# Optimization experiments

Measured on AMD Instinct MI355X. Metric: run time of the kernel, lower is better.

The kernel has to match this reference:

```python
import jax, jax.numpy as jnp
import numpy as np

B, L, DIN, DH, DE = 16, 128, 768, 300, 100
ALPHA = 0.2
NEG = -9e15


def setup_inputs() -> dict:
    key = jax.random.key(0)
    k = jax.random.split(key, 7)
    s = lambda fan: 1.0 / np.sqrt(fan)
    return {
        "x": jax.random.normal(k[0], (B, L, DIN), jnp.float32),
        "adj": jax.random.randint(k[1], (B, L, L), 0, 2, jnp.int32),
        "edge_embedding": jax.random.normal(k[2], (B, L, L, DE), jnp.float32),
        "W": jax.random.normal(k[3], (DIN, DH), jnp.float32) * s(DIN),
        "a": jax.random.normal(k[4], (2 * DH, 1), jnp.float32) * s(2 * DH),
        "edge_map_w": jax.random.normal(k[5], (DH, DE), jnp.float32) * s(DE),
        "edge_map_b": jnp.zeros((DH,), jnp.float32),
        "edge_lin_w": jax.random.normal(k[6], (1, DH), jnp.float32) * s(DH),
        "edge_lin_b": jnp.zeros((1,), jnp.float32),
    }


def _forward(x, edge_embedding, W, a, edge_map_w, edge_map_b, edge_lin_w, edge_lin_b, adj):
    h = x @ W  # [B, L, DH]
    # Faithful to torch: h.repeat_interleave(L, dim=2).view(B, L*L, DH) scrambles
    # features: a_input_first[b, i*L+j, d] = h[b, i, (j*DH + d) // L].
    # So e1[b,i,j] = sum_d h[b,i,(j*DH+d)//L] * a[d] = h[b,i] . V[j], with V[j,k] =
    # sum of a[d] over d where (j*DH+d)//L == k. Build V once by scatter-add.
    idx = (jnp.arange(L)[:, None] * DH + jnp.arange(DH)[None, :]) // L  # [L, DH], values in [0, DH)
    a_first = a[:DH, 0]
    V = jnp.zeros((L, DH), h.dtype).at[jnp.arange(L)[:, None], idx].add(a_first[None, :])  # [L, DH]
    e1 = jnp.einsum('bik,jk->bij', h, V)  # [B, L, L]
    # Second half: h.repeat_interleave(L, dim=0).view(...) gives plain h_j tiling.
    e2 = h @ a[DH:, 0]  # [B, L], broadcast over i
    e = jax.nn.leaky_relu(e1 + e2[:, None, :], ALPHA)  # [B, L, L]
    # Edge-weight gate (use_edge_weight == 'yes'); note torch relu result is discarded.
    em = edge_embedding @ edge_map_w.T + edge_map_b  # [B, L, L, DH]
    ew = jax.nn.sigmoid(em @ edge_lin_w.T + edge_lin_b)[..., 0]  # [B, L, L]
    e_final = e * ew
    att = jax.nn.softmax(jnp.where(adj > 0, e_final, NEG), axis=2)  # dropout off (eval)
    return h + jnp.matmul(att, h)  # residual add, concat=False


def reference(x, adj, edge_embedding, W, a, edge_map_w, edge_map_b, edge_lin_w, edge_lin_b):
    return _forward(x, edge_embedding, W, a, edge_map_w, edge_map_b, edge_lin_w, edge_lin_b, adj)
```

## Files before the change

kernel.cpp:

```cpp
#include <hip/hip_runtime.h>
#include <hip/hip_bf16.h>


#define L 128
#define DH 300
#define DIN 768
#define DE 100
#define KSL 4
#define MROWS 2048

__global__ __launch_bounds__(256) void k_small(
    const float* __restrict__ A,
    const float* __restrict__ EMW,
    const float* __restrict__ EMB,
    const float* __restrict__ ELW,
    const float* __restrict__ ELB,
    float* __restrict__ CV, float* __restrict__ C0,
    float* __restrict__ VW, int* __restrict__ VCOL)
{
    int t = threadIdx.x;
    if (blockIdx.x == 0) {
        if (t < DE) {
            float s = 0.f;
            for (int k = 0; k < DH; ++k)
                s += ELW[k] * EMW[k * DE + t];
            CV[t] = s;
        } else if (t == DE) {
            float s = 0.f;
            for (int k = 0; k < DH; ++k)
                s += ELW[k] * EMB[k];
            C0[0] = s + ELB[0];
        }
    } else {
        if (t < L) {
            int base = t * DH;
            int cm = base >> 7;
            float w0 = 0.f, w1 = 0.f, w2 = 0.f, w3 = 0.f;
            for (int j = 0; j < DH; ++j) {
                int u = ((base + j) >> 7) - cm;
                float av = A[j];
                w0 += (u == 0) ? av : 0.f;
                w1 += (u == 1) ? av : 0.f;
                w2 += (u == 2) ? av : 0.f;
                w3 += (u == 3) ? av : 0.f;
            }
            VCOL[t] = cm;
            VW[t * 4 + 0] = w0; VW[t * 4 + 1] = w1;
            VW[t * 4 + 2] = w2; VW[t * 4 + 3] = w3;
        }
    }
}

__global__ __launch_bounds__(256) void k_gemm(
    const float* __restrict__ X,
    const float* __restrict__ Wm,
    float* __restrict__ HP)
{
    __shared__ float As[32 * 33];
    __shared__ float Bs[32 * 80];
    int t = threadIdx.x;
    int ty = t >> 4, tx = t & 15;
    int r0 = blockIdx.y * 32;
    int c0 = blockIdx.x * 80;
    int kbase = blockIdx.z * (DIN / KSL);

    float acc[2][5];
#pragma unroll
    for (int r = 0; r < 2; ++r)
#pragma unroll
        for (int c = 0; c < 5; ++c) acc[r][c] = 0.f;

    for (int ks = 0; ks < DIN / KSL; ks += 32) {
        int kk = kbase + ks;
#pragma unroll
        for (int s = 0; s < 4; ++s) {
            int idx = t + 256 * s;
            int row = idx >> 5, k = idx & 31;
            As[k * 33 + row] = X[(size_t)(r0 + row) * DIN + kk + k];
        }
        for (int idx = t; idx < 640; idx += 256) {
            int k = idx / 20, c4 = idx % 20;
            int c = c4 * 4;
            int col = c0 + c;
            float4 v;
            if (col + 3 < DH) v = *(const float4*)(Wm + (size_t)(kk + k) * DH + col);
            else { v.x = 0.f; v.y = 0.f; v.z = 0.f; v.w = 0.f; }
            *(float4*)(Bs + k * 80 + c) = v;
        }
        __syncthreads();
#pragma unroll
        for (int k = 0; k < 32; ++k) {
            float av0 = As[k * 33 + ty * 2];
            float av1 = As[k * 33 + ty * 2 + 1];
            float bv[5];
#pragma unroll
            for (int c = 0; c < 5; ++c) bv[c] = Bs[k * 80 + tx * 5 + c];
#pragma unroll
            for (int c = 0; c < 5; ++c) {
                acc[0][c] = fmaf(av0, bv[c], acc[0][c]);
                acc[1][c] = fmaf(av1, bv[c], acc[1][c]);
            }
        }
        __syncthreads();
    }
    float* out = HP + (size_t)blockIdx.z * (MROWS * DH);
#pragma unroll
    for (int r = 0; r < 2; ++r) {
        int row = r0 + ty * 2 + r;
#pragma unroll
        for (int c = 0; c < 5; ++c) {
            int col = c0 + tx * 5 + c;
            if (col < DH) out[(size_t)row * DH + col] = acc[r][c];
        }
    }
}

__global__ __launch_bounds__(256) void k_red(
    const float* __restrict__ HP, const float* __restrict__ A,
    float* __restrict__ H, float* __restrict__ E2)
{
    const size_t SL = (size_t)MROWS * DH;
    int t = threadIdx.x;
    int row = blockIdx.x * 8 + (t >> 5);
    int lane = t & 31;
    const float4* p0 = (const float4*)(HP + (size_t)row * DH);
    const float4* p1 = (const float4*)(HP + SL + (size_t)row * DH);
    const float4* p2 = (const float4*)(HP + 2 * SL + (size_t)row * DH);
    const float4* p3 = (const float4*)(HP + 3 * SL + (size_t)row * DH);
    const float4* a4 = (const float4*)(A + DH);
    float4* hout = (float4*)(H + (size_t)row * DH);
    float acc = 0.f;
    for (int k4 = lane; k4 < DH / 4; k4 += 32) {
        float4 v0 = p0[k4], v1 = p1[k4], v2 = p2[k4], v3 = p3[k4];
        float4 av = a4[k4];
        float4 hv;
        hv.x = (v0.x + v1.x) + (v2.x + v3.x);
        hv.y = (v0.y + v1.y) + (v2.y + v3.y);
        hv.z = (v0.z + v1.z) + (v2.z + v3.z);
        hv.w = (v0.w + v1.w) + (v2.w + v3.w);
        hout[k4] = hv;
        acc += hv.x * av.x + hv.y * av.y + hv.z * av.z + hv.w * av.w;
    }
#pragma unroll
    for (int o = 16; o >= 1; o >>= 1) acc += __shfl_xor(acc, o);
    if (lane == 0) E2[row] = acc;
}

__global__ __launch_bounds__(256) void k_attn(
    const float* __restrict__ EE,
    const int* __restrict__ ADJ,
    const float* __restrict__ H,
    const float* __restrict__ E2,
    const float* __restrict__ CV, const float* __restrict__ C0,
    const float* __restrict__ VW, const int* __restrict__ VCOL,
    float* __restrict__ OUT)
{
    __shared__ float hrow[DH];
    __shared__ float cl[DE];
    __shared__ float ef[L];
    __shared__ float att[L];
    __shared__ float red[4];

    int bid = blockIdx.x;
    int b = bid >> 7;
    int t = threadIdx.x;

    for (int k = t; k < DH; k += 256) hrow[k] = H[(size_t)bid * DH + k];
    if (t < DE) cl[t] = CV[t];
    __syncthreads();

    {
        int j = t >> 1, half = t & 1;
        const float2* p = (const float2*)(EE + (size_t)bid * (L * DE) + j * DE + half * 50);
        const float* cp = cl + half * 50;
        float s = 0.f;
#pragma unroll
        for (int q = 0; q < 25; ++q) {
            float2 v = p[q];
            s = fmaf(v.x, cp[2 * q], s);
            s = fmaf(v.y, cp[2 * q + 1], s);
        }
        s += __shfl_xor(s, 1);
        float ewv = 1.f / (1.f + expf(-(s + C0[0])));

        int cm = VCOL[j];
        float e1 = 0.f;
#pragma unroll
        for (int u = 0; u < 4; ++u) {
            int c = cm + u; if (c > DH - 1) c = DH - 1;
            e1 += VW[j * 4 + u] * hrow[c];
        }
        float e = e1 + E2[(size_t)b * L + j];
        e = (e > 0.f) ? e : 0.2f * e;
        float efv = (ADJ[(size_t)bid * L + j] > 0) ? e * ewv : -9.0e15f;
        if (half == 0) ef[j] = efv;
    }
    __syncthreads();

    float v = (t < L) ? ef[t] : -3.0e38f;
#pragma unroll
    for (int o = 32; o >= 1; o >>= 1) v = fmaxf(v, __shfl_xor(v, o));
    int wid = t >> 6;
    if ((t & 63) == 0) red[wid] = v;
    __syncthreads();
    float mx = fmaxf(fmaxf(red[0], red[1]), fmaxf(red[2], red[3]));
    __syncthreads();
    float p = (t < L) ? expf(ef[t] - mx) : 0.f;
    v = p;
#pragma unroll
    for (int o = 32; o >= 1; o >>= 1) v += __shfl_xor(v, o);
    if ((t & 63) == 0) red[wid] = v;
    __syncthreads();
    float denom = red[0] + red[1] + red[2] + red[3];
    if (t < L) att[t] = p / denom;
    __syncthreads();

    const float* Hb = H + (size_t)b * L * DH;
    for (int k = t; k < DH; k += 256) {
        float a0 = hrow[k], a1 = 0.f, a2 = 0.f, a3 = 0.f;
#pragma unroll 4
        for (int j = 0; j < L; j += 4) {
            a0 = fmaf(att[j + 0], Hb[(size_t)(j + 0) * DH + k], a0);
            a1 = fmaf(att[j + 1], Hb[(size_t)(j + 1) * DH + k], a1);
            a2 = fmaf(att[j + 2], Hb[(size_t)(j + 2) * DH + k], a2);
            a3 = fmaf(att[j + 3], Hb[(size_t)(j + 3) * DH + k], a3);
        }
        OUT[(size_t)bid * DH + k] = (a0 + a1) + (a2 + a3);
    }
}

extern "C" void kernel_launch(void* const* d_in, const int* in_sizes, int n_in,
                              void* d_out, int out_size, void* d_ws, size_t ws_size,
                              hipStream_t stream) {
    const float* X   = (const float*)d_in[0];
    const int*   ADJ = (const int*)d_in[1];
    const float* EE  = (const float*)d_in[2];
    const float* Wm  = (const float*)d_in[3];
    const float* A   = (const float*)d_in[4];
    const float* EMW = (const float*)d_in[5];
    const float* EMB = (const float*)d_in[6];
    const float* ELW = (const float*)d_in[7];
    const float* ELB = (const float*)d_in[8];
    float* OUT = (float*)d_out;

    float* ws = (float*)d_ws;
    float* HP   = ws;
    float* H    = ws + 2457600;
    float* E2   = ws + 3072000;
    float* CV   = ws + 3074048;
    float* C0   = ws + 3074148;
    float* VW   = ws + 3074152;
    int*   VCOL = (int*)(ws + 3074664);

    k_small<<<dim3(2), dim3(256), 0, stream>>>(A, EMW, EMB, ELW, ELB, CV, C0, VW, VCOL);
    k_gemm<<<dim3(4, 64, 4), dim3(256), 0, stream>>>(X, Wm, HP);
    k_red<<<dim3(256), dim3(256), 0, stream>>>(HP, A, H, E2);
    k_attn<<<dim3(2048), dim3(256), 0, stream>>>(EE, ADJ, H, E2, CV, C0, VW, VCOL, OUT);
}
```

Baseline: 87.98 us.

## Compute x@W with bf16 MFMA using pre-transposed bf16 weights

Replaces the scalar fp32 split-K GEMM with a bf16 MFMA 16x16x32 kernel on 64x64 tiles. A new kernel transposes W and converts it to bf16 each call, and X is converted to bf16 while it is staged into shared memory. The aim is to use the matrix cores instead of FMA loops, at the cost of one extra launch and lower precision for h, which then feeds the attention scores and the output.

```diff
diff --git a/kernel.cpp b/kernel.cpp
--- a/kernel.cpp
+++ b/kernel.cpp
@@ -6,8 +6,20 @@
 #define DH 300
 #define DIN 768
 #define DE 100
-#define KSL 4
+#define SPLITK 4
 #define MROWS 2048
+#define SL ((size_t)MROWS * DH)
+
+typedef __bf16 bf16x8 __attribute__((ext_vector_type(8)));
+typedef float f32x4 __attribute__((ext_vector_type(4)));
+typedef unsigned short ushort_t;
+
+__device__ __forceinline__ ushort_t f2bf(float f) {
+    __bf16 h = (__bf16)f;
+    ushort_t u;
+    __builtin_memcpy(&u, &h, 2);
+    return u;
+}
 
 __global__ __launch_bounds__(256) void k_small(
     const float* __restrict__ A,
@@ -51,66 +63,92 @@
     }
 }
 
+__global__ __launch_bounds__(256) void k_cvt(
+    const float* __restrict__ Wm, ushort_t* __restrict__ WT)
+{
+    __shared__ float tile[64][65];
+    int k0 = blockIdx.x * 64;
+    int c0 = blockIdx.y * 64;
+    int t = threadIdx.x;
+#pragma unroll
+    for (int s = 0; s < 16; ++s) {
+        int idx = t + 256 * s;
+        int kr = idx >> 6, cc = idx & 63;
+        int c = c0 + cc;
+        tile[kr][cc] = (c < DH) ? Wm[(size_t)(k0 + kr) * DH + c] : 0.f;
+    }
+    __syncthreads();
+#pragma unroll
+    for (int s = 0; s < 16; ++s) {
+        int idx = t + 256 * s;
+        int c = idx >> 6, kr = idx & 63;
+        WT[(size_t)(c0 + c) * DIN + k0 + kr] = f2bf(tile[kr][c]);
+    }
+}
+
 __global__ __launch_bounds__(256) void k_gemm(
     const float* __restrict__ X,
-    const float* __restrict__ Wm,
+    const ushort_t* __restrict__ WT,
     float* __restrict__ HP)
 {
-    __shared__ float As[32 * 33];
-    __shared__ float Bs[32 * 80];
-    int t = threadIdx.x;
-    int ty = t >> 4, tx = t & 15;
-    int r0 = blockIdx.y * 32;
-    int c0 = blockIdx.x * 80;
-    int kbase = blockIdx.z * (DIN / KSL);
-
-    float acc[2][5];
-#pragma unroll
-    for (int r = 0; r < 2; ++r)
-#pragma unroll
-        for (int c = 0; c < 5; ++c) acc[r][c] = 0.f;
-
-    for (int ks = 0; ks < DIN / KSL; ks += 32) {
-        int kk = kbase + ks;
-#pragma unroll
-        for (int s = 0; s < 4; ++s) {
-            int idx = t + 256 * s;
-            int row = idx >> 5, k = idx & 31;
-            As[k * 33 + row] = X[(size_t)(r0 + row) * DIN + kk + k];
-        }
-        for (int idx = t; idx < 640; idx += 256) {
-            int k = idx / 20, c4 = idx % 20;
-            int c = c4 * 4;
-            int col = c0 + c;
-            float4 v;
-            if (col + 3 < DH) v = *(const float4*)(Wm + (size_t)(kk + k) * DH + col);
-            else { v.x = 0.f; v.y = 0.f; v.z = 0.f; v.w = 0.f; }
-            *(float4*)(Bs + k * 80 + c) = v;
+    __shared__ ushort_t As[64 * 72];
+    __shared__ ushort_t Bs[64 * 72];
+    int t = threadIdx.x;
+    int w = t >> 6;
+    int lane = t & 63;
+    int lr = lane & 15;
+    int lk = lane >> 4;
+    int r0 = blockIdx.y * 64;
+    int c0 = blockIdx.x * 64;
+    int kbase = blockIdx.z * (DIN / SPLITK);
+
+    f32x4 acc[4];
+#pragma unroll
+    for (int ct = 0; ct < 4; ++ct) acc[ct] = (f32x4){0.f, 0.f, 0.f, 0.f};
+
+    int srow = t >> 2, skq = (t & 3) * 16;
+
+    for (int step = 0; step < 3; ++step) {
+        int kk = kbase + step * 64;
+        {
+            const float4* xs = (const float4*)(X + (size_t)(r0 + srow) * DIN + kk + skq);
+            float4 f0 = xs[0], f1 = xs[1], f2 = xs[2], f3 = xs[3];
+            bf16x8 v0, v1;
+            v0[0] = (__bf16)f0.x; v0[1] = (__bf16)f0.y; v0[2] = (__bf16)f0.z; v0[3] = (__bf16)f0.w;
+            v0[4] = (__bf16)f1.x; v0[5] = (__bf16)f1.y; v0[6] = (__bf16)f1.z; v0[7] = (__bf16)f1.w;
+            v1[0] = (__bf16)f2.x; v1[1] = (__bf16)f2.y; v1[2] = (__bf16)f2.z; v1[3] = (__bf16)f2.w;
+            v1[4] = (__bf16)f3.x; v1[5] = (__bf16)f3.y; v1[6] = (__bf16)f3.z; v1[7] = (__bf16)f3.w;
+            *(bf16x8*)&As[srow * 72 + skq] = v0;
+            *(bf16x8*)&As[srow * 72 + skq + 8] = v1;
+        }
+        {
+            const uint4* wp = (const uint4*)(WT + (size_t)(c0 + srow) * DIN + kk + skq);
+            uint4 u0 = wp[0], u1 = wp[1];
+            *(uint4*)&Bs[srow * 72 + skq] = u0;
+            *(uint4*)&Bs[srow * 72 + skq + 8] = u1;
         }
         __syncthreads();
 #pragma unroll
-        for (int k = 0; k < 32; ++k) {
-            float av0 = As[k * 33 + ty * 2];
-            float av1 = As[k * 33 + ty * 2 + 1];
-            float bv[5];
-#pragma unroll
-            for (int c = 0; c < 5; ++c) bv[c] = Bs[k * 80 + tx * 5 + c];
-#pragma unroll
-            for (int c = 0; c < 5; ++c) {
-                acc[0][c] = fmaf(av0, bv[c], acc[0][c]);
-                acc[1][c] = fmaf(av1, bv[c], acc[1][c]);
+        for (int k2 = 0; k2 < 2; ++k2) {
+            bf16x8 af = *(bf16x8*)&As[(w * 16 + lr) * 72 + k2 * 32 + lk * 8];
+#pragma unroll
+            for (int ct = 0; ct < 4; ++ct) {
+                bf16x8 bf_ = *(bf16x8*)&Bs[(ct * 16 + lr) * 72 + k2 * 32 + lk * 8];
+                acc[ct] = __builtin_amdgcn_mfma_f32_16x16x32_bf16(af, bf_, acc[ct], 0, 0, 0);
             }
         }
         __syncthreads();
     }
-    float* out = HP + (size_t)blockIdx.z * (MROWS * DH);
-#pragma unroll
-    for (int r = 0; r < 2; ++r) {
-        int row = r0 + ty * 2 + r;
-#pragma unroll
-        for (int c = 0; c < 5; ++c) {
-            int col = c0 + tx * 5 + c;
-            if (col < DH) out[(size_t)row * DH + col] = acc[r][c];
+    float* outp = HP + (size_t)blockIdx.z * SL;
+#pragma unroll
+    for (int ct = 0; ct < 4; ++ct) {
+        int col = c0 + ct * 16 + lr;
+        if (col < DH) {
+#pragma unroll
+            for (int r = 0; r < 4; ++r) {
+                int row = r0 + w * 16 + lk * 4 + r;
+                outp[(size_t)row * DH + col] = acc[ct][r];
+            }
         }
     }
 }
@@ -119,25 +157,20 @@
     const float* __restrict__ HP, const float* __restrict__ A,
     float* __restrict__ H, float* __restrict__ E2)
 {
-    const size_t SL = (size_t)MROWS * DH;
     int t = threadIdx.x;
     int row = blockIdx.x * 8 + (t >> 5);
     int lane = t & 31;
-    const float4* p0 = (const float4*)(HP + (size_t)row * DH);
-    const float4* p1 = (const float4*)(HP + SL + (size_t)row * DH);
-    const float4* p2 = (const float4*)(HP + 2 * SL + (size_t)row * DH);
-    const float4* p3 = (const float4*)(HP + 3 * SL + (size_t)row * DH);
     const float4* a4 = (const float4*)(A + DH);
     float4* hout = (float4*)(H + (size_t)row * DH);
     float acc = 0.f;
     for (int k4 = lane; k4 < DH / 4; k4 += 32) {
-        float4 v0 = p0[k4], v1 = p1[k4], v2 = p2[k4], v3 = p3[k4];
+        float4 hv; hv.x = 0.f; hv.y = 0.f; hv.z = 0.f; hv.w = 0.f;
+#pragma unroll
+        for (int z = 0; z < SPLITK; ++z) {
+            float4 v = ((const float4*)(HP + (size_t)z * SL + (size_t)row * DH))[k4];
+            hv.x += v.x; hv.y += v.y; hv.z += v.z; hv.w += v.w;
+        }
         float4 av = a4[k4];
-        float4 hv;
-        hv.x = (v0.x + v1.x) + (v2.x + v3.x);
-        hv.y = (v0.y + v1.y) + (v2.y + v3.y);
-        hv.z = (v0.z + v1.z) + (v2.z + v3.z);
-        hv.w = (v0.w + v1.w) + (v2.w + v3.w);
         hout[k4] = hv;
         acc += hv.x * av.x + hv.y * av.y + hv.z * av.z + hv.w * av.w;
     }
@@ -251,9 +284,11 @@
     float* C0   = ws + 3074148;
     float* VW   = ws + 3074152;
     int*   VCOL = (int*)(ws + 3074664);
+    ushort_t* WT = (ushort_t*)(ws + 3074816);
 
     k_small<<<dim3(2), dim3(256), 0, stream>>>(A, EMW, EMB, ELW, ELB, CV, C0, VW, VCOL);
-    k_gemm<<<dim3(4, 64, 4), dim3(256), 0, stream>>>(X, Wm, HP);
+    k_cvt<<<dim3(12, 5), dim3(256), 0, stream>>>(Wm, WT);
+    k_gemm<<<dim3(5, 32, SPLITK), dim3(256), 0, stream>>>(X, WT, HP);
     k_red<<<dim3(256), dim3(256), 0, stream>>>(HP, A, H, E2);
     k_attn<<<dim3(2048), dim3(256), 0, stream>>>(EE, ADJ, H, E2, CV, C0, VW, VCOL, OUT);
 }
```

Measured after the change: 72.68 us. -17.4%, faster.
